# Kernel tuning notes

Hardware: AMD Instinct MI355X
Metric: run time of the kernel (lower is better)

Reference implementation:

```python
import jax, jax.numpy as jnp
import numpy as np

N_USERS = 100000
N_ITEMS = 50000
N_NODES = N_USERS + N_ITEMS
NNZ = 4800000
EMB = 64
N_LAYERS = 3
BATCH = 4096
REG = 1e-5


def setup_inputs() -> dict:
    key = jax.random.key(0)
    ks = jax.random.split(key, 12)
    rows = jax.random.randint(ks[0], (NNZ,), 0, N_NODES, dtype=jnp.int32)
    cols = jax.random.randint(ks[1], (NNZ,), 0, N_NODES, dtype=jnp.int32)
    # normalized-Laplacian-like positive edge weights
    vals = jax.random.uniform(ks[2], (NNZ,), dtype=jnp.float32) * 0.05
    user_emb = jax.random.normal(ks[3], (N_USERS, EMB), dtype=jnp.float32) * 0.1
    item_emb = jax.random.normal(ks[4], (N_ITEMS, EMB), dtype=jnp.float32) * 0.1
    # xavier-ish scale for 64x64: std ~= 0.125
    W_one = jax.random.normal(ks[5], (N_LAYERS, EMB, EMB), dtype=jnp.float32) * 0.125
    b_one = jax.random.normal(ks[6], (N_LAYERS, EMB), dtype=jnp.float32) * 0.125
    W_two = jax.random.normal(ks[7], (N_LAYERS, EMB, EMB), dtype=jnp.float32) * 0.125
    b_two = jax.random.normal(ks[8], (N_LAYERS, EMB), dtype=jnp.float32) * 0.125
    u = jax.random.randint(ks[9], (BATCH,), 0, N_USERS, dtype=jnp.int32)
    i = jax.random.randint(ks[10], (BATCH,), 0, N_ITEMS, dtype=jnp.int32)
    j = jax.random.randint(ks[11], (BATCH,), 0, N_ITEMS, dtype=jnp.int32)
    return {"rows": rows, "cols": cols, "vals": vals, "user_emb": user_emb,
            "item_emb": item_emb, "W_one": W_one, "b_one": b_one,
            "W_two": W_two, "b_two": b_two, "u": u, "i": i, "j": j}


def _spmm(rows, cols, vals, x):
    # sparse.mm(L, x): gather rows of x at cols, scale by edge vals, scatter-add into rows
    return jax.ops.segment_sum(vals[:, None] * x[cols], rows, num_segments=N_NODES)


def reference(rows, cols, vals, user_emb, item_emb, W_one, b_one, W_two, b_two, u, i, j):
    ego = jnp.concatenate([user_emb, item_emb], axis=0)  # [N_NODES, EMB]
    finals = [ego]
    for k in range(N_LAYERS):
        xk = finals[k]
        side_L = _spmm(rows, cols, vals, xk)          # L @ x
        side_LI = side_L + xk                          # (L + I) @ x
        simple = side_LI @ W_one[k] + b_one[k]
        interaction = (side_L * xk) @ W_two[k] + b_two[k]
        ego_k = jax.nn.leaky_relu(simple + interaction)  # mess_dropout=0 -> identity
        norm = ego_k / jnp.maximum(jnp.linalg.norm(ego_k, axis=1, keepdims=True), 1e-12)
        finals.append(norm)
    final = jnp.concatenate(finals, axis=1)            # [N_NODES, EMB*(1+N_LAYERS)]
    u_emb = final[u]
    p_emb = final[N_USERS + i]
    n_emb = final[N_USERS + j]
    y_ui = jnp.sum(u_emb * p_emb, axis=1)
    y_uj = jnp.sum(u_emb * n_emb, axis=1)
    bpr_loss = -jnp.mean(jax.nn.log_sigmoid(y_ui - y_uj))
    l2norm = (jnp.sum(u_emb ** 2) / 2.0 + jnp.sum(p_emb ** 2) / 2.0 + jnp.sum(n_emb ** 2) / 2.0) / BATCH
    return bpr_loss + REG * l2norm
```

## Files before the change

### kernel.cpp

```cpp
#include <hip/hip_runtime.h>
#include <hip/hip_bf16.h>
#include <math.h>

#define N_USERS 100000
#define N_ITEMS 50000
#define N_NODES 150000
#define NNZ     4800000
#define EMB     64
#define BATCH   4096
#define REG_C   1e-5f

#define ROWB    512
#define NBK     293
#define PADC    17408
#define CSTRIDE 16
#define P1_EPB  4096
#define NB_P1   ((NNZ + P1_EPB - 1) / P1_EPB)
#define NB_PACK 2344
#define NB_ACC0 1024

#define LROW    36

typedef short short8 __attribute__((ext_vector_type(8)));
typedef float f32x4  __attribute__((ext_vector_type(4)));
typedef float f32x2  __attribute__((ext_vector_type(2)));

static __device__ __forceinline__ unsigned short f2bf(float f) {
    unsigned u = __float_as_uint(f);
    u = u + 0x7FFFu + ((u >> 16) & 1u);
    return (unsigned short)(u >> 16);
}
static __device__ __forceinline__ unsigned pk2(float lo, float hi) {
    return (unsigned)f2bf(lo) | ((unsigned)f2bf(hi) << 16);
}
static __device__ __forceinline__ float blo(unsigned a) { return __uint_as_float(a << 16); }
static __device__ __forceinline__ float bhi(unsigned a) { return __uint_as_float(a & 0xFFFF0000u); }

static __device__ __forceinline__ unsigned pkq4(float f0, float f1, float f2, float f3) {
    int v = __builtin_amdgcn_cvt_pk_fp8_f32(f0, f1, 0, false);
    v = __builtin_amdgcn_cvt_pk_fp8_f32(f2, f3, v, true);
    return (unsigned)v;
}

static __device__ __forceinline__ void eload(const int2* p_, int& c, float& v) {
    unsigned long long w = __builtin_nontemporal_load((const unsigned long long*)p_);
    c = (int)(unsigned)(w & 0xFFFFFFFFu);
    v = __int_as_float((int)(unsigned)(w >> 32));
}
static __device__ __forceinline__ int ntl(const int* p_) {
    return __builtin_nontemporal_load(p_);
}
static __device__ __forceinline__ float ntlf(const float* p_) {
    return __builtin_nontemporal_load(p_);
}

__global__ __launch_bounds__(256) void p1_bin_kernel(
    const int* __restrict__ rows, const int* __restrict__ cols,
    const float* __restrict__ vals, int* __restrict__ gcursor,
    int2* __restrict__ binned,
    const float* __restrict__ ue, const float* __restrict__ ie,
    unsigned int* __restrict__ xh, unsigned int* __restrict__ xq,
    const int* __restrict__ u, const int* __restrict__ ii,
    const int* __restrict__ jj,
    float* __restrict__ dui, float* __restrict__ duj, float* __restrict__ l2a) {
    __shared__ int2 staged[P1_EPB];
    __shared__ int hist[NBK];
    __shared__ int lofs[NBK];
    __shared__ int baseg[NBK];
    __shared__ int scanx[512];
    int t = threadIdx.x;
    int bid = blockIdx.x;

    if (bid >= NB_P1 + NB_PACK) {
        int b = (bid - NB_P1 - NB_PACK) * 4 + (t >> 6);
        int lane = t & 63;
        float uv = ue[(size_t)u[b] * 64 + lane];
        float pv = ie[(size_t)ii[b] * 64 + lane];
        float nv = ie[(size_t)jj[b] * 64 + lane];
        float a = uv * pv, c = uv * nv, l = uv * uv + pv * pv + nv * nv;
        #pragma unroll
        for (int o = 32; o > 0; o >>= 1) {
            a += __shfl_xor(a, o, 64);
            c += __shfl_xor(c, o, 64);
            l += __shfl_xor(l, o, 64);
        }
        if (lane == 0) { dui[b] = a; duj[b] = c; l2a[b] = l; }
        return;
    }
    if (bid >= NB_P1) {
        int g0 = ((bid - NB_P1) * 256 + t) * 2;
        #pragma unroll
        for (int g = g0; g < g0 + 2; ++g) {
            if (g >= N_NODES * 8) break;
            const float4* src;
            if (g < N_USERS * 8) src = (const float4*)ue + (size_t)g * 2;
            else src = (const float4*)ie + (size_t)(g - N_USERS * 8) * 2;
            float4 a = src[0], b = src[1];
            uint4 h;
            h.x = pk2(a.x, a.y); h.y = pk2(a.z, a.w);
            h.z = pk2(b.x, b.y); h.w = pk2(b.z, b.w);
            ((uint4*)xh)[g] = h;
            uint2 q;
            q.x = pkq4(a.x, a.y, a.z, a.w);
            q.y = pkq4(b.x, b.y, b.z, b.w);
            ((uint2*)xq)[g] = q;
        }
        return;
    }

    int e0 = bid * P1_EPB;
    int nE = NNZ - e0; if (nE > P1_EPB) nE = P1_EPB;

    for (int b = t; b < NBK; b += 256) hist[b] = 0;
    __syncthreads();
    for (int i = t; i < nE; i += 256) atomicAdd(&hist[rows[e0 + i] >> 9], 1);
    __syncthreads();

    scanx[t]       = (t < NBK) ? hist[t] : 0;
    scanx[t + 256] = (t + 256 < NBK) ? hist[t + 256] : 0;
    __syncthreads();
    for (int o = 1; o < 512; o <<= 1) {
        int i1 = t + 256;
        int v0 = (t >= o) ? scanx[t - o] : 0;
        int v1 = (i1 >= o) ? scanx[i1 - o] : 0;
        __syncthreads();
        scanx[t] += v0; scanx[i1] += v1;
        __syncthreads();
    }
    for (int b = t; b < NBK; b += 256) {
        int h = hist[b];
        lofs[b]  = scanx[b] - h;
        baseg[b] = (h > 0) ? atomicAdd(&gcursor[b * CSTRIDE], h) : 0;
        hist[b]  = 0;
    }
    __syncthreads();

    for (int i = t; i < nE; i += 256) {
        int r = rows[e0 + i];
        int b = r >> 9;
        int slot = lofs[b] + atomicAdd(&hist[b], 1);
        staged[slot] = make_int2(ntl(&cols[e0 + i]) | ((r & 511) << 18),
                                 __float_as_int(ntlf(&vals[e0 + i])));
    }
    __syncthreads();

    for (int s = t; s < nE; s += 256) {
        int2 rec = staged[s];
        int lo = 0, hi = NBK - 1;
        while (lo < hi) {
            int mid = (lo + hi + 1) >> 1;
            if (lofs[mid] <= s) lo = mid; else hi = mid - 1;
        }
        int rel = baseg[lo] + (s - lofs[lo]);
        if (rel < PADC)
            binned[(size_t)lo * PADC + rel] = rec;
    }
}

__global__ __launch_bounds__(256) void p2_sort_kernel(
    const int* __restrict__ gcursor, const int2* __restrict__ binned,
    int2* __restrict__ csr, int* __restrict__ start, int* __restrict__ cnt) {
    __shared__ int hist[ROWB];
    __shared__ int excl[ROWB];
    int b = blockIdx.x;
    int t = threadIdx.x;
    size_t bbase = (size_t)b * PADC;
    int n = gcursor[b * CSTRIDE];
    if (n > PADC) n = PADC;
    hist[t] = 0; hist[t + 256] = 0;
    __syncthreads();
    for (int i = t; i < n; i += 256)
        atomicAdd(&hist[(binned[bbase + i].x >> 18) & 511], 1);
    __syncthreads();
    excl[t] = hist[t]; excl[t + 256] = hist[t + 256];
    __syncthreads();
    for (int o = 1; o < ROWB; o <<= 1) {
        int i1 = t + 256;
        int v0 = (t >= o) ? excl[t - o] : 0;
        int v1 = (i1 >= o) ? excl[i1 - o] : 0;
        __syncthreads();
        excl[t] += v0; excl[i1] += v1;
        __syncthreads();
    }
    int rowsInB = N_NODES - b * ROWB;
    if (rowsInB > ROWB) rowsInB = ROWB;
    for (int rr = t; rr < ROWB; rr += 256) {
        int s = excl[rr] - hist[rr];
        if (rr < rowsInB) {
            start[b * ROWB + rr] = (int)bbase + s;
            cnt[b * ROWB + rr]   = hist[rr];
        }
        excl[rr] = s;
    }
    __syncthreads();
    for (int i = t; i < n; i += 256) {
        int2 rec = binned[bbase + i];
        int rl = (rec.x >> 18) & 511;
        int p = atomicAdd(&excl[rl], 1);
        csr[bbase + p] = make_int2(rec.x & 0x3FFFF, rec.y);
    }
}

__global__ __launch_bounds__(256) void spmm_csr_kernel(
    const int* __restrict__ start, const int* __restrict__ cnt,
    const int2* __restrict__ edges, const unsigned int* __restrict__ xq,
    unsigned int* __restrict__ out) {
    int row = blockIdx.x * 4 + (threadIdx.x >> 6);
    if (row >= N_NODES) return;
    int lane = threadIdx.x & 63;
    int eg = lane >> 4;
    int p  = lane & 15;
    int s = start[row];
    int n = cnt[row];
    float a0 = 0.f, a1 = 0.f, a2 = 0.f, a3 = 0.f;
    int k = 0;
    for (; k + 32 <= n; k += 32) {
        int c[8]; float v[8];
        #pragma unroll
        for (int j = 0; j < 8; ++j) eload(&edges[s + k + 4 * j + eg], c[j], v[j]);
        #pragma unroll
        for (int j = 0; j < 8; ++j) {
            unsigned q = xq[(size_t)c[j] * 16 + p];
            f32x2 lo = __builtin_amdgcn_cvt_pk_f32_fp8(q, false);
            f32x2 hi = __builtin_amdgcn_cvt_pk_f32_fp8(q, true);
            a0 = fmaf(v[j], lo[0], a0);
            a1 = fmaf(v[j], lo[1], a1);
            a2 = fmaf(v[j], hi[0], a2);
            a3 = fmaf(v[j], hi[1], a3);
        }
    }
    while (k < n) {
        #pragma unroll
        for (int j = 0; j < 4; ++j) {
            int off = k + 4 * j + eg;
            bool valid = off < n;
            int c; float v;
            eload(&edges[s + (valid ? off : 0)], c, v);
            if (!valid) v = 0.f;
            unsigned q = xq[(size_t)c * 16 + p];
            f32x2 lo = __builtin_amdgcn_cvt_pk_f32_fp8(q, false);
            f32x2 hi = __builtin_amdgcn_cvt_pk_f32_fp8(q, true);
            a0 = fmaf(v, lo[0], a0);
            a1 = fmaf(v, lo[1], a1);
            a2 = fmaf(v, hi[0], a2);
            a3 = fmaf(v, hi[1], a3);
        }
        k += 16;
    }
    a0 += __shfl_xor(a0, 16, 64); a0 += __shfl_xor(a0, 32, 64);
    a1 += __shfl_xor(a1, 16, 64); a1 += __shfl_xor(a1, 32, 64);
    a2 += __shfl_xor(a2, 16, 64); a2 += __shfl_xor(a2, 32, 64);
    a3 += __shfl_xor(a3, 16, 64); a3 += __shfl_xor(a3, 32, 64);
    if (eg == 0) {
        uint2 o2;
        o2.x = pk2(a0, a1);
        o2.y = pk2(a2, a3);
        ((uint2*)out)[(size_t)row * 16 + p] = o2;
    }
}

__global__ __launch_bounds__(256) void dense_kernel(
    unsigned int* xh, unsigned int* xq, const unsigned int* __restrict__ sideL,
    const float* __restrict__ W1, const float* __restrict__ b1,
    const float* __restrict__ W2, const float* __restrict__ b2)
{
    __shared__ unsigned asl[64 * LROW];
    __shared__ unsigned apr[64 * LROW];
    __shared__ unsigned wt1[64 * LROW];
    __shared__ unsigned wt2[64 * LROW];

    int t = threadIdx.x;
    int r0 = blockIdx.x * 64;

    #pragma unroll
    for (int i = 0; i < 4; ++i) {
        int idx = i * 256 + t;
        int kk = idx >> 4;
        int ng = idx & 15;
        float4 w1v = ((const float4*)W1)[idx];
        float4 w2v = ((const float4*)W2)[idx];
        unsigned short* s1 = (unsigned short*)wt1;
        unsigned short* s2 = (unsigned short*)wt2;
        int c0 = 4 * ng;
        s1[(c0 + 0) * (2 * LROW) + kk] = f2bf(w1v.x);
        s1[(c0 + 1) * (2 * LROW) + kk] = f2bf(w1v.y);
        s1[(c0 + 2) * (2 * LROW) + kk] = f2bf(w1v.z);
        s1[(c0 + 3) * (2 * LROW) + kk] = f2bf(w1v.w);
        s2[(c0 + 0) * (2 * LROW) + kk] = f2bf(w2v.x);
        s2[(c0 + 1) * (2 * LROW) + kk] = f2bf(w2v.y);
        s2[(c0 + 2) * (2 * LROW) + kk] = f2bf(w2v.z);
        s2[(c0 + 3) * (2 * LROW) + kk] = f2bf(w2v.w);
    }

    #pragma unroll
    for (int i = 0; i < 2; ++i) {
        int q = i * 256 + t;
        int row = q >> 3;
        int u4 = q & 7;
        uint4 h  = make_uint4(0, 0, 0, 0);
        uint4 sb = make_uint4(0, 0, 0, 0);
        if (r0 + row < N_NODES) {
            h  = ((const uint4*)xh)[(size_t)(r0 + row) * 8 + u4];
            sb = ((const uint4*)sideL)[(size_t)(r0 + row) * 8 + u4];
        }
        float x0 = blo(h.x), x1 = bhi(h.x), x2 = blo(h.y), x3 = bhi(h.y);
        float x4 = blo(h.z), x5 = bhi(h.z), x6 = blo(h.w), x7 = bhi(h.w);
        float d0 = blo(sb.x), d1 = bhi(sb.x), d2 = blo(sb.y), d3 = bhi(sb.y);
        float d4 = blo(sb.z), d5 = bhi(sb.z), d6 = blo(sb.w), d7 = bhi(sb.w);
        uint4 sa, pa;
        sa.x = pk2(x0 + d0, x1 + d1); sa.y = pk2(x2 + d2, x3 + d3);
        sa.z = pk2(x4 + d4, x5 + d5); sa.w = pk2(x6 + d6, x7 + d7);
        pa.x = pk2(x0 * d0, x1 * d1); pa.y = pk2(x2 * d2, x3 * d3);
        pa.z = pk2(x4 * d4, x5 * d5); pa.w = pk2(x6 * d6, x7 * d7);
        *(uint4*)&asl[row * LROW + 4 * u4] = sa;
        *(uint4*)&apr[row * LROW + 4 * u4] = pa;
    }
    __syncthreads();

    int l = t & 63, wv = t >> 6;
    int q4 = l >> 4, mr = l & 15;
    int abase = (wv * 16 + mr) * LROW + 4 * q4;
    short8 aS0 = *(const short8*)&asl[abase];
    short8 aS1 = *(const short8*)&asl[abase + 16];
    short8 aP0 = *(const short8*)&apr[abase];
    short8 aP1 = *(const short8*)&apr[abase + 16];

    float lr[4][4];
    float rowss[4] = {0.f, 0.f, 0.f, 0.f};
    #pragma unroll
    for (int nb = 0; nb < 4; ++nb) {
        int wbase = (nb * 16 + mr) * LROW + 4 * q4;
        short8 b10 = *(const short8*)&wt1[wbase];
        short8 b11 = *(const short8*)&wt1[wbase + 16];
        short8 b20 = *(const short8*)&wt2[wbase];
        short8 b21 = *(const short8*)&wt2[wbase + 16];
        f32x4 acc = {0.f, 0.f, 0.f, 0.f};
        acc = __builtin_amdgcn_mfma_f32_16x16x32_bf16(aS0, b10, acc, 0, 0, 0);
        acc = __builtin_amdgcn_mfma_f32_16x16x32_bf16(aS1, b11, acc, 0, 0, 0);
        acc = __builtin_amdgcn_mfma_f32_16x16x32_bf16(aP0, b20, acc, 0, 0, 0);
        acc = __builtin_amdgcn_mfma_f32_16x16x32_bf16(aP1, b21, acc, 0, 0, 0);
        float bias = b1[nb * 16 + mr] + b2[nb * 16 + mr];
        #pragma unroll
        for (int r = 0; r < 4; ++r) {
            float v = acc[r] + bias;
            float lrv = v > 0.f ? v : 0.01f * v;
            lr[nb][r] = lrv;
            rowss[r] += lrv * lrv;
        }
    }
    #pragma unroll
    for (int o = 1; o < 16; o <<= 1) {
        #pragma unroll
        for (int r = 0; r < 4; ++r) rowss[r] += __shfl_xor(rowss[r], o, 64);
    }
    float inv[4];
    #pragma unroll
    for (int r = 0; r < 4; ++r) inv[r] = 1.f / fmaxf(sqrtf(rowss[r]), 1e-12f);

    __syncthreads();
    unsigned short* os = (unsigned short*)wt1;
    #pragma unroll
    for (int nb = 0; nb < 4; ++nb) {
        #pragma unroll
        for (int r = 0; r < 4; ++r) {
            int rloc = wv * 16 + q4 * 4 + r;
            os[rloc * (2 * LROW) + nb * 16 + mr] = f2bf(lr[nb][r] * inv[r]);
        }
    }
    __syncthreads();

    #pragma unroll
    for (int i = 0; i < 2; ++i) {
        int q = i * 256 + t;
        int row = q >> 3, u4 = q & 7;
        if (r0 + row < N_NODES) {
            uint4 h = *(const uint4*)&wt1[row * LROW + 4 * u4];
            ((uint4*)xh)[(size_t)(r0 + row) * 8 + u4] = h;
            uint2 qq;
            qq.x = pkq4(blo(h.x), bhi(h.x), blo(h.y), bhi(h.y));
            qq.y = pkq4(blo(h.z), bhi(h.z), blo(h.w), bhi(h.w));
            ((uint2*)xq)[(size_t)(r0 + row) * 8 + u4] = qq;
        }
    }
}

__global__ void accB_kernel(const unsigned int* __restrict__ xh,
                            const int* __restrict__ u, const int* __restrict__ ii,
                            const int* __restrict__ jj,
                            float* __restrict__ dui, float* __restrict__ duj,
                            float* __restrict__ l2a) {
    int t = threadIdx.x;
    int lane = t & 63;
    int half = lane >> 5, p = lane & 31;
    int b = blockIdx.x * 8 + (t >> 6) * 2 + half;
    unsigned ua = xh[(size_t)u[b] * 32 + p];
    unsigned pa = xh[(size_t)(N_USERS + ii[b]) * 32 + p];
    unsigned na = xh[(size_t)(N_USERS + jj[b]) * 32 + p];
    float u0 = blo(ua), u1 = bhi(ua);
    float p0 = blo(pa), p1 = bhi(pa);
    float n0 = blo(na), n1 = bhi(na);
    float a = u0 * p0 + u1 * p1;
    float c = u0 * n0 + u1 * n1;
    float l = u0 * u0 + u1 * u1 + p0 * p0 + p1 * p1 + n0 * n0 + n1 * n1;
    #pragma unroll
    for (int o = 16; o > 0; o >>= 1) {
        a += __shfl_xor(a, o, 64);
        c += __shfl_xor(c, o, 64);
        l += __shfl_xor(l, o, 64);
    }
    if (p == 0) { dui[b] += a; duj[b] += c; l2a[b] += l; }
}

__global__ void final_kernel(const float* __restrict__ dui, const float* __restrict__ duj,
                             const float* __restrict__ l2a, float* __restrict__ out) {
    __shared__ float sh[4];
    int t = threadIdx.x;
    float s = 0.f;
    for (int b = t; b < BATCH; b += 256) {
        float diff = dui[b] - duj[b];
        float ls = (diff >= 0.f) ? -log1pf(expf(-diff)) : (diff - log1pf(expf(diff)));
        s += -ls + REG_C * 0.5f * l2a[b];
    }
    #pragma unroll
    for (int o = 32; o > 0; o >>= 1) s += __shfl_xor(s, o, 64);
    int wave = t >> 6, lane = t & 63;
    if (lane == 0) sh[wave] = s;
    __syncthreads();
    if (t == 0) out[0] = (sh[0] + sh[1] + sh[2] + sh[3]) / (float)BATCH;
}

extern "C" void kernel_launch(void* const* d_in, const int* in_sizes, int n_in,
                              void* d_out, int out_size, void* d_ws, size_t ws_size,
                              hipStream_t stream) {
    const int*   rows     = (const int*)d_in[0];
    const int*   cols     = (const int*)d_in[1];
    const float* vals     = (const float*)d_in[2];
    const float* user_emb = (const float*)d_in[3];
    const float* item_emb = (const float*)d_in[4];
    const float* W_one    = (const float*)d_in[5];
    const float* b_one    = (const float*)d_in[6];
    const float* W_two    = (const float*)d_in[7];
    const float* b_two    = (const float*)d_in[8];
    const int*   u        = (const int*)d_in[9];
    const int*   ii       = (const int*)d_in[10];
    const int*   jj       = (const int*)d_in[11];

    unsigned int* Xh  = (unsigned int*)d_ws;
    unsigned int* Xq  = Xh + (size_t)N_NODES * 32;
    int2* binned      = (int2*)(Xq + (size_t)N_NODES * 16);
    unsigned int* B   = (unsigned int*)binned;
    int2* csr         = binned + (size_t)NBK * PADC;
    int*  gcursor     = (int*)(csr + (size_t)NBK * PADC);
    int*  startA      = gcursor + NBK * CSTRIDE;
    int*  cntA        = startA + 150016;
    float* dui        = (float*)(cntA + 150016);
    float* duj        = dui + BATCH;
    float* l2a        = duj + BATCH;

    (void)hipMemsetAsync(gcursor, 0, NBK * CSTRIDE * sizeof(int), stream);

    p1_bin_kernel<<<NB_P1 + NB_PACK + NB_ACC0, 256, 0, stream>>>(
        rows, cols, vals, gcursor, binned,
        user_emb, item_emb, Xh, Xq, u, ii, jj, dui, duj, l2a);
    p2_sort_kernel<<<NBK, 256, 0, stream>>>(gcursor, binned, csr, startA, cntA);

    for (int k = 0; k < 3; ++k) {
        spmm_csr_kernel<<<(N_NODES + 3) / 4, 256, 0, stream>>>(startA, cntA, csr, Xq, B);
        dense_kernel<<<(N_NODES + 63) / 64, 256, 0, stream>>>(
            Xh, Xq, B, W_one + k * 4096, b_one + k * 64,
            W_two + k * 4096, b_two + k * 64);
        accB_kernel<<<BATCH / 8, 256, 0, stream>>>(Xh, u, ii, jj, dui, duj, l2a);
    }

    final_kernel<<<1, 256, 0, stream>>>(dui, duj, l2a, (float*)d_out);
}
```

Measured before the change: 634.6 us.

## Use wave-shuffle scans and bucket tags in CSR build, widen sort blocks

The binning kernel replaces its shared-memory Hillis-Steele scan over buckets with a single-wave shuffle scan and issues the global cursor atomics before the scan so they overlap it. It also stores a per-slot bucket byte so the scatter pass no longer needs a binary search. The row-sort kernel moves to 1024-thread blocks and a two-level shuffle scan, and all barriers become a custom LDS-only wait plus s_barrier. Together these cut barrier count and latency in the preprocessing kernels. The custom barrier only waits on LDS counters, so correctness depends on no global-memory ordering being needed across those points.

```diff
diff --git a/kernel.cpp b/kernel.cpp
--- a/kernel.cpp
+++ b/kernel.cpp
@@ -52,6 +52,13 @@
 }
 static __device__ __forceinline__ float ntlf(const float* p_) {
     return __builtin_nontemporal_load(p_);
+}
+
+static __device__ __forceinline__ void ldsbar() {
+    __builtin_amdgcn_sched_barrier(0);
+    asm volatile("s_waitcnt lgkmcnt(0)" ::: "memory");
+    __builtin_amdgcn_s_barrier();
+    __builtin_amdgcn_sched_barrier(0);
 }
 
 __global__ __launch_bounds__(256) void p1_bin_kernel(
@@ -64,10 +71,10 @@
     const int* __restrict__ jj,
     float* __restrict__ dui, float* __restrict__ duj, float* __restrict__ l2a) {
     __shared__ int2 staged[P1_EPB];
+    __shared__ unsigned char bkt[P1_EPB];
     __shared__ int hist[NBK];
     __shared__ int lofs[NBK];
     __shared__ int baseg[NBK];
-    __shared__ int scanx[512];
     int t = threadIdx.x;
     int bid = blockIdx.x;
 
@@ -110,90 +117,103 @@
 
     int e0 = bid * P1_EPB;
     int nE = NNZ - e0; if (nE > P1_EPB) nE = P1_EPB;
+    int wv = t >> 6, l = t & 63;
 
     for (int b = t; b < NBK; b += 256) hist[b] = 0;
-    __syncthreads();
+    ldsbar();
     for (int i = t; i < nE; i += 256) atomicAdd(&hist[rows[e0 + i] >> 9], 1);
-    __syncthreads();
-
-    scanx[t]       = (t < NBK) ? hist[t] : 0;
-    scanx[t + 256] = (t + 256 < NBK) ? hist[t + 256] : 0;
-    __syncthreads();
-    for (int o = 1; o < 512; o <<= 1) {
-        int i1 = t + 256;
-        int v0 = (t >= o) ? scanx[t - o] : 0;
-        int v1 = (i1 >= o) ? scanx[i1 - o] : 0;
-        __syncthreads();
-        scanx[t] += v0; scanx[i1] += v1;
-        __syncthreads();
-    }
-    for (int b = t; b < NBK; b += 256) {
-        int h = hist[b];
-        lofs[b]  = scanx[b] - h;
-        baseg[b] = (h > 0) ? atomicAdd(&gcursor[b * CSTRIDE], h) : 0;
-        hist[b]  = 0;
-    }
-    __syncthreads();
+    ldsbar();
+
+    int bA = t, bB = t + 256;
+    int hA = (bA < NBK) ? hist[bA] : 0;
+    int hB = (bB < NBK) ? hist[bB] : 0;
+    int resA = 0, resB = 0;
+    if (hA > 0) resA = atomicAdd(&gcursor[bA * CSTRIDE], hA);
+    if (hB > 0) resB = atomicAdd(&gcursor[bB * CSTRIDE], hB);
+    if (wv == 0) {
+        int carry = 0;
+        #pragma unroll
+        for (int c = 0; c < 5; ++c) {
+            int idx = c * 64 + l;
+            int v = (idx < NBK) ? hist[idx] : 0;
+            int x = v;
+            #pragma unroll
+            for (int o = 1; o < 64; o <<= 1) {
+                int y = __shfl_up(x, o, 64);
+                if (l >= o) x += y;
+            }
+            if (idx < NBK) lofs[idx] = carry + x - v;
+            carry += __shfl(x, 63, 64);
+        }
+    }
+    ldsbar();
 
     for (int i = t; i < nE; i += 256) {
         int r = rows[e0 + i];
-        int b = r >> 9;
-        int slot = lofs[b] + atomicAdd(&hist[b], 1);
+        int bb = r >> 9;
+        int rk = atomicAdd(&hist[bb], -1);
+        int slot = lofs[bb] + rk - 1;
         staged[slot] = make_int2(ntl(&cols[e0 + i]) | ((r & 511) << 18),
                                  __float_as_int(ntlf(&vals[e0 + i])));
-    }
-    __syncthreads();
-
+        bkt[slot] = (unsigned char)bb;
+    }
+    if (bA < NBK) baseg[bA] = resA;
+    if (bB < NBK) baseg[bB] = resB;
+    ldsbar();
+
+    int L256 = lofs[256];
     for (int s = t; s < nE; s += 256) {
         int2 rec = staged[s];
-        int lo = 0, hi = NBK - 1;
-        while (lo < hi) {
-            int mid = (lo + hi + 1) >> 1;
-            if (lofs[mid] <= s) lo = mid; else hi = mid - 1;
-        }
-        int rel = baseg[lo] + (s - lofs[lo]);
+        int bb = (int)bkt[s] + ((s >= L256) ? 256 : 0);
+        int rel = baseg[bb] + (s - lofs[bb]);
         if (rel < PADC)
-            binned[(size_t)lo * PADC + rel] = rec;
-    }
-}
-
-__global__ __launch_bounds__(256) void p2_sort_kernel(
+            binned[(size_t)bb * PADC + rel] = rec;
+    }
+}
+
+__global__ __launch_bounds__(1024) void p2_sort_kernel(
     const int* __restrict__ gcursor, const int2* __restrict__ binned,
     int2* __restrict__ csr, int* __restrict__ start, int* __restrict__ cnt) {
     __shared__ int hist[ROWB];
     __shared__ int excl[ROWB];
+    __shared__ int chunk[8];
     int b = blockIdx.x;
     int t = threadIdx.x;
+    int wv = t >> 6, l = t & 63;
     size_t bbase = (size_t)b * PADC;
     int n = gcursor[b * CSTRIDE];
     if (n > PADC) n = PADC;
-    hist[t] = 0; hist[t + 256] = 0;
-    __syncthreads();
-    for (int i = t; i < n; i += 256)
+    if (t < ROWB) hist[t] = 0;
+    ldsbar();
+    for (int i = t; i < n; i += 1024)
         atomicAdd(&hist[(binned[bbase + i].x >> 18) & 511], 1);
-    __syncthreads();
-    excl[t] = hist[t]; excl[t + 256] = hist[t + 256];
-    __syncthreads();
-    for (int o = 1; o < ROWB; o <<= 1) {
-        int i1 = t + 256;
-        int v0 = (t >= o) ? excl[t - o] : 0;
-        int v1 = (i1 >= o) ? excl[i1 - o] : 0;
-        __syncthreads();
-        excl[t] += v0; excl[i1] += v1;
-        __syncthreads();
-    }
-    int rowsInB = N_NODES - b * ROWB;
-    if (rowsInB > ROWB) rowsInB = ROWB;
-    for (int rr = t; rr < ROWB; rr += 256) {
-        int s = excl[rr] - hist[rr];
-        if (rr < rowsInB) {
-            start[b * ROWB + rr] = (int)bbase + s;
-            cnt[b * ROWB + rr]   = hist[rr];
-        }
-        excl[rr] = s;
-    }
-    __syncthreads();
-    for (int i = t; i < n; i += 256) {
+    ldsbar();
+    int incl = 0;
+    if (t < ROWB) {
+        incl = hist[t];
+        #pragma unroll
+        for (int o = 1; o < 64; o <<= 1) {
+            int y = __shfl_up(incl, o, 64);
+            if (l >= o) incl += y;
+        }
+        if (l == 63) chunk[wv] = incl;
+    }
+    ldsbar();
+    if (t < ROWB) {
+        int add = 0;
+        #pragma unroll
+        for (int c = 0; c < 8; ++c) add += (c < wv) ? chunk[c] : 0;
+        int s = incl + add - hist[t];
+        int rowsInB = N_NODES - b * ROWB;
+        if (rowsInB > ROWB) rowsInB = ROWB;
+        if (t < rowsInB) {
+            start[b * ROWB + t] = (int)bbase + s;
+            cnt[b * ROWB + t]   = hist[t];
+        }
+        excl[t] = s;
+    }
+    ldsbar();
+    for (int i = t; i < n; i += 1024) {
         int2 rec = binned[bbase + i];
         int rl = (rec.x >> 18) & 511;
         int p = atomicAdd(&excl[rl], 1);
@@ -462,7 +482,7 @@
     p1_bin_kernel<<<NB_P1 + NB_PACK + NB_ACC0, 256, 0, stream>>>(
         rows, cols, vals, gcursor, binned,
         user_emb, item_emb, Xh, Xq, u, ii, jj, dui, duj, l2a);
-    p2_sort_kernel<<<NBK, 256, 0, stream>>>(gcursor, binned, csr, startA, cntA);
+    p2_sort_kernel<<<NBK, 1024, 0, stream>>>(gcursor, binned, csr, startA, cntA);
 
     for (int k = 0; k < 3; ++k) {
         spmm_csr_kernel<<<(N_NODES + 3) / 4, 256, 0, stream>>>(startA, cntA, csr, Xq, B);
```

Result: faster. 601.0 us (-5.3%).
